# Performance work log

Hardware: AMD Instinct MI355X
Metric: run time of the kernel (lower is better)

Reference implementation:

```python
import jax, jax.numpy as jnp
import numpy as np

C, INTER, RED4 = 256, 128, 64  # in_channels, inter_ch=max(C//2,32), C//4

def setup_inputs() -> dict:
    key = jax.random.key(0)
    ks = jax.random.split(key, 12)
    B, H, W = 8, 64, 64
    s = 0.02
    return {
        "x": jax.random.normal(ks[0], (B, C, H, W), dtype=jnp.float32),
        "theta_w": jax.random.normal(ks[1], (INTER, C), dtype=jnp.float32) * s,
        "phi_w": jax.random.normal(ks[2], (INTER, C), dtype=jnp.float32) * s,
        "g_w": jax.random.normal(ks[3], (INTER, C), dtype=jnp.float32) * s,
        "out_w": jax.random.normal(ks[4], (C, INTER), dtype=jnp.float32) * s,
        "bn_gamma": jnp.ones((C,), dtype=jnp.float32),
        "bn_beta": jnp.zeros((C,), dtype=jnp.float32),
        "fc1_w": jax.random.normal(ks[5], (RED4, C), dtype=jnp.float32) * s,
        "fc1_b": jnp.zeros((RED4,), dtype=jnp.float32),
        "fc2_w": jax.random.normal(ks[6], (C, RED4), dtype=jnp.float32) * s,
        "fc2_b": jnp.zeros((C,), dtype=jnp.float32),
    }

def reference(x, theta_w, phi_w, g_w, out_w, bn_gamma, bn_beta, fc1_w, fc1_b, fc2_w, fc2_b):
    B, Cc, H, W = x.shape
    N = H * W
    xf = x.reshape(B, Cc, N)                              # [B,C,N]
    # 1x1 convs == per-pixel matmuls
    theta = jnp.einsum('ic,bcn->bni', theta_w, xf)        # [B,N,I]
    phi = jnp.einsum('ic,bcn->bin', phi_w, xf)            # [B,I,N]
    g = jnp.einsum('ic,bcn->bni', g_w, xf)                # [B,N,I]
    scale = 1.0 / jnp.sqrt(jnp.asarray(theta.shape[-1], theta.dtype))
    attn = jax.nn.softmax(jnp.einsum('bni,bim->bnm', theta, phi) * scale, axis=-1)  # [B,N,N]
    out = jnp.einsum('bnm,bmi->bni', attn, g)             # [B,N,I]
    out = jnp.einsum('ci,bni->bcn', out_w, out).reshape(B, Cc, H, W)
    # BatchNorm2d (training mode: batch stats, biased variance, eps=1e-5)
    mean = out.mean(axis=(0, 2, 3))
    var = out.var(axis=(0, 2, 3))
    out = (out - mean[:, None, None]) * jax.lax.rsqrt(var[:, None, None] + 1e-5)
    out = out * bn_gamma[:, None, None] + bn_beta[:, None, None]
    # SE channel attention on the input x
    pooled = x.mean(axis=(2, 3))                          # [B,C]
    h = jax.nn.relu(pooled @ fc1_w.T + fc1_b)
    ch_w = jax.nn.sigmoid(h @ fc2_w.T + fc2_b)[:, :, None, None]
    return x + out * ch_w
```

## Files before the change

### kernel.cpp

```cpp
#include <hip/hip_runtime.h>

#define B_DIM 8
#define C_DIM 256
#define I_DIM 128
#define N_DIM 4096
#define R_DIM 64

typedef unsigned short u16;
typedef unsigned int u32;
typedef __attribute__((ext_vector_type(8))) __bf16 bf16x8;
typedef __attribute__((ext_vector_type(4))) float f32x4;
typedef __attribute__((ext_vector_type(16))) float f32x16;

union BF8 { u32 u[4]; bf16x8 v; };

__device__ __forceinline__ u16 f2bf(float f) {
    union { float f; u32 u; } v; v.f = f;
    u32 r = v.u + 0x7FFFu + ((v.u >> 16) & 1u);
    return (u16)(r >> 16);
}
__device__ __forceinline__ float bf2f(u16 h) {
    union { u32 u; float f; } v; v.u = (u32)h << 16; return v.f;
}
__device__ __forceinline__ u32 pk2(float a, float b) {
    return (u32)f2bf(a) | ((u32)f2bf(b) << 16);
}
__device__ __forceinline__ u32 pk2t(float a, float b) {
    union { float f; u32 u; } ua, ub; ua.f = a; ub.f = b;
    return __builtin_amdgcn_perm(ub.u, ua.u, 0x07060302u);
}
__device__ __forceinline__ void async16(const u16* g, u16* l) {
    __builtin_amdgcn_global_load_lds((const __attribute__((address_space(1))) void*)g,
                                     (__attribute__((address_space(3))) void*)l, 16, 0, 0);
}
__device__ __forceinline__ void plswap(u32& a, u32& b) {
    __asm__("v_permlane32_swap_b32 %0, %1" : "+v"(a), "+v"(b));
}

#define TH_SCALE 0.1275204890136f

static constexpr size_t OFF_BNSUM = 0;
static constexpr size_t OFF_BNSQ  = 1024;
static constexpr size_t OFF_POOL  = 2048;
static constexpr size_t OFF_CHW   = 10240;
static constexpr size_t OFF_W3    = 18432;
static constexpr size_t OFF_OWB   = 215040;
static constexpr size_t OFF_AO0   = 280576;
static constexpr size_t OFF_AO1   = OFF_AO0 + 8388608;
static constexpr size_t OFF_THETA = OFF_AO1 + 8388608;
static constexpr size_t OFF_PHIT  = OFF_THETA + 8388608;
static constexpr size_t OFF_GT    = OFF_PHIT + 8388608;
static constexpr size_t OFF_L0    = OFF_GT + 8388608;
static constexpr size_t OFF_L1    = OFF_L0 + 131072;
static constexpr size_t OFF_OUT2  = OFF_L1 + 131072;

__global__ void prep_kernel(const float* __restrict__ tw, const float* __restrict__ pw,
                            const float* __restrict__ gw, const float* __restrict__ ow,
                            u16* __restrict__ w3, u16* __restrict__ owb,
                            float* __restrict__ bnzero, float* __restrict__ pooled) {
    int idx = blockIdx.x * 256 + threadIdx.x;
    if (idx < 512) bnzero[idx] = 0.f;
    if (idx < 2048) pooled[idx] = 0.f;
    if (idx < 3 * 32768) {
        const float* src = idx < 32768 ? tw : (idx < 65536 ? pw : gw);
        w3[idx] = f2bf(src[idx & 32767]);
    }
    if (idx < 32768) owb[idx] = f2bf(ow[idx]);
}

__global__ __launch_bounds__(256) void qkv_kernel(const float* __restrict__ x,
                                                  const u16* __restrict__ w3,
                                                  u16* __restrict__ theta,
                                                  u16* __restrict__ phiT,
                                                  u16* __restrict__ gT,
                                                  float* __restrict__ pooled) {
    const int bid = blockIdx.x;
    const int b = bid & 7, nt = bid >> 3;
    const int n0 = nt * 64;
    const int t = threadIdx.x, lane = t & 63, w = t >> 6;
    const int cl = lane & 31, h = lane >> 5;

    __shared__ u16 As[64 * 256];
    __shared__ u16 Ep[128 * 72];

    {
        const float* xb = x + ((size_t)b * C_DIM) * N_DIM + n0;
        for (int it = 0; it < 16; ++it) {
            int id = it * 256 + t;
            int c = id >> 4, l16 = id & 15;
            float4 v = *(const float4*)(xb + (size_t)c * N_DIM + l16 * 4);
            int g = c >> 3, co = c & 7;
            float vv[4] = {v.x, v.y, v.z, v.w};
            #pragma unroll
            for (int k = 0; k < 4; ++k) {
                int n = l16 * 4 + k;
                As[n * 256 + ((g ^ (n & 7)) << 3) + co] = f2bf(vv[k]);
            }
            float s = (v.x + v.y) + (v.z + v.w);
            s += __shfl_xor(s, 1); s += __shfl_xor(s, 2);
            s += __shfl_xor(s, 4); s += __shfl_xor(s, 8);
            if ((t & 15) == 0) atomicAdd(&pooled[b * C_DIM + c], s);
        }
    }
    __syncthreads();

    const int mt = w & 1;
    const int ip = w >> 1;
    bf16x8 afr[16];
    #pragma unroll
    for (int ks = 0; ks < 16; ++ks) {
        int r = mt * 32 + cl;
        int g = 2 * ks + h;
        afr[ks] = *(const bf16x8*)&As[r * 256 + ((g ^ (r & 7)) << 3)];
    }

    for (int z = 0; z < 3; ++z) {
        const u16* wz = w3 + z * (I_DIM * C_DIM);
        f32x16 acc[2] = {};
        #pragma unroll
        for (int ks = 0; ks < 16; ++ks) {
            #pragma unroll
            for (int f = 0; f < 2; ++f) {
                int irow = (2 * ip + f) * 32 + cl;
                bf16x8 bfr = *(const bf16x8*)(wz + (size_t)irow * C_DIM + ks * 16 + h * 8);
                acc[f] = __builtin_amdgcn_mfma_f32_32x32x16_bf16(afr[ks], bfr, acc[f], 0, 0, 0);
            }
        }
        if (z < 2) {
            float sc = (z == 0) ? TH_SCALE : 1.0f;
            #pragma unroll
            for (int f = 0; f < 2; ++f) {
                int i = (2 * ip + f) * 32 + cl;
                #pragma unroll
                for (int r2 = 0; r2 < 4; ++r2)
                    #pragma unroll
                    for (int e = 0; e < 4; ++e) {
                        int n = mt * 32 + 8 * r2 + 4 * h + e;
                        Ep[n * 136 + i] = f2bf(acc[f][4 * r2 + e] * sc);
                    }
            }
            __syncthreads();
            u16* dst = (z == 0) ? theta : phiT;
            #pragma unroll
            for (int it = 0; it < 4; ++it) {
                int id = it * 256 + t;
                int n = id >> 4, l16 = id & 15;
                f32x4 vv = *(const f32x4*)&Ep[n * 136 + l16 * 8];
                *(f32x4*)(dst + ((size_t)(b * N_DIM) + n0 + n) * I_DIM + l16 * 8) = vv;
            }
            __syncthreads();
        } else {
            #pragma unroll
            for (int f = 0; f < 2; ++f) {
                int i = (2 * ip + f) * 32 + cl;
                #pragma unroll
                for (int r2 = 0; r2 < 4; ++r2) {
                    u32 lo = pk2(acc[f][4 * r2 + 0], acc[f][4 * r2 + 1]);
                    u32 hi = pk2(acc[f][4 * r2 + 2], acc[f][4 * r2 + 3]);
                    int nb = mt * 32 + 8 * r2 + 4 * h;
                    *(u32*)&Ep[i * 72 + nb] = lo;
                    *(u32*)&Ep[i * 72 + nb + 2] = hi;
                }
            }
            __syncthreads();
            #pragma unroll
            for (int it = 0; it < 4; ++it) {
                int id = it * 256 + t;
                int i = id >> 3, l8 = id & 7;
                f32x4 vv = *(const f32x4*)&Ep[i * 72 + l8 * 8];
                *(f32x4*)(gT + ((size_t)(b * I_DIM) + i) * N_DIM + n0 + l8 * 8) = vv;
            }
        }
    }
}

__global__ __launch_bounds__(512, 2) void attn_kernel(const u16* __restrict__ theta,
                                                      const u16* __restrict__ phiT,
                                                      const u16* __restrict__ gT,
                                                      u16* __restrict__ ao0, u16* __restrict__ ao1,
                                                      float* __restrict__ l0, float* __restrict__ l1,
                                                      const float* __restrict__ pooled,
                                                      const float* __restrict__ fc1w,
                                                      const float* __restrict__ fc1b,
                                                      const float* __restrict__ fc2w,
                                                      const float* __restrict__ fc2b,
                                                      float* __restrict__ chw) {
    const int bid = blockIdx.x;
    const int b = bid & 7, mh = (bid >> 3) & 1, qt = bid >> 4;
    const int t = threadIdx.x, lane = t & 63, w = t >> 6;
    const int cl = lane & 31, h = lane >> 5;
    const int wt = w & 3, kh = w >> 2;
    const int qw = qt * 128 + wt * 32;

    __shared__ __align__(16) u16 SM[34816];
    __shared__ float lexs[8][32];
    __shared__ float sse[512];

    bf16x8 qf[8];
    {
        const u16* qp = theta + ((size_t)(b * N_DIM) + qw + cl) * I_DIM + h * 8;
        #pragma unroll
        for (int ks = 0; ks < 8; ++ks) qf[ks] = *(const bf16x8*)(qp + ks * 16);
    }

    const u16* kbase = phiT + (size_t)b * N_DIM * I_DIM + (size_t)(mh * 2048) * I_DIM;
    const u16* vbase = gT + (size_t)b * I_DIM * N_DIM + mh * 2048;
    const u16* kptr[2]; const u16* vptr[2];
    #pragma unroll
    for (int it = 0; it < 2; ++it) {
        int gi = (w * 2 + it) * 64 + lane;
        int kr = gi >> 4, kg = gi & 15;
        kptr[it] = kbase + (size_t)kr * I_DIM + ((kg ^ (kr & 7)) << 3);
        int vr = gi >> 3, vg = gi & 7;
        vptr[it] = vbase + (size_t)vr * N_DIM + ((vg ^ (vr & 7)) << 3);
    }

    auto issue = [&](int p) {
        u16* Kd = SM + p * 16384;
        u16* Vd = Kd + 8192;
        #pragma unroll
        for (int it = 0; it < 2; ++it) { async16(kptr[it], Kd + (w * 2 + it) * 512); kptr[it] += 64 * I_DIM; }
        #pragma unroll
        for (int it = 0; it < 2; ++it) { async16(vptr[it], Vd + (w * 2 + it) * 512); vptr[it] += 64; }
    };

    float lsum = 0.f;
    f32x16 O[4] = {};
    const int krow = kh * 32 + cl;
    const int kswz = krow & 7;

    issue(0);

    for (int mc = 0; mc < 32; ++mc) {
        const int p = mc & 1;
        __asm__ volatile("s_barrier" ::: "memory");
        if (mc < 31) {
            issue(1 - p);
            __asm__ volatile("s_waitcnt vmcnt(4)" ::: "memory");
        } else {
            __asm__ volatile("s_waitcnt vmcnt(0)" ::: "memory");
        }
        __asm__ volatile("s_barrier" ::: "memory");

        const u16* Ks = SM + p * 16384;
        const u16* Vs = Ks + 8192;

        f32x16 S = {};
        __builtin_amdgcn_s_setprio(1);
        #pragma unroll
        for (int ks = 0; ks < 8; ++ks) {
            bf16x8 kf = *(const bf16x8*)&Ks[krow * 128 + (((2 * ks + h) ^ kswz) << 3)];
            S = __builtin_amdgcn_mfma_f32_32x32x16_bf16(kf, qf[ks], S, 0, 0, 0);
        }
        __builtin_amdgcn_s_setprio(0);

        u32 pk[4][2];
        #pragma unroll
        for (int r2 = 0; r2 < 4; ++r2) {
            float p0 = __builtin_amdgcn_exp2f(S[4 * r2 + 0]);
            float p1 = __builtin_amdgcn_exp2f(S[4 * r2 + 1]);
            float p2 = __builtin_amdgcn_exp2f(S[4 * r2 + 2]);
            float p3 = __builtin_amdgcn_exp2f(S[4 * r2 + 3]);
            lsum += (p0 + p1) + (p2 + p3);
            pk[r2][0] = pk2t(p0, p1);
            pk[r2][1] = pk2t(p2, p3);
        }

        __builtin_amdgcn_s_setprio(1);
        #pragma unroll
        for (int s = 0; s < 2; ++s) {
            u32 x0 = pk[2 * s][0], y0 = pk[2 * s + 1][0];
            u32 x1 = pk[2 * s][1], y1 = pk[2 * s + 1][1];
            plswap(x0, y0);
            plswap(x1, y1);
            BF8 A;
            A.u[0] = x0; A.u[1] = x1; A.u[2] = y0; A.u[3] = y1;
            const int g = 4 * kh + 2 * s + h;
            #pragma unroll
            for (int f = 0; f < 4; ++f) {
                int ir = f * 32 + cl;
                bf16x8 vf = *(const bf16x8*)&Vs[ir * 64 + ((g ^ (ir & 7)) << 3)];
                O[f] = __builtin_amdgcn_mfma_f32_32x32x16_bf16(A.v, vf, O[f], 0, 0, 0);
            }
        }
        __builtin_amdgcn_s_setprio(0);
    }

    {
        union { float f; u32 u; } a, b2;
        a.f = lsum; b2.f = lsum;
        plswap(a.u, b2.u);
        lsum = a.f + b2.f;
    }
    if (h == 0) lexs[w][cl] = lsum;
    __syncthreads();

    float* ep32 = (float*)SM;
    float* slot = ep32 + ((wt << 6) + lane) * 68;
    if (kh == 0) {
        #pragma unroll
        for (int f = 0; f < 4; ++f)
            #pragma unroll
            for (int r2 = 0; r2 < 4; ++r2) {
                f32x4 vv = {O[f][4 * r2 + 0], O[f][4 * r2 + 1], O[f][4 * r2 + 2], O[f][4 * r2 + 3]};
                *(f32x4*)(slot + f * 16 + r2 * 4) = vv;
            }
    }
    __syncthreads();

    u16* aop = (mh == 0) ? ao0 : ao1;
    float* lp = (mh == 0) ? l0 : l1;

    if (kh == 1) {
        if (h == 0) lp[(size_t)b * N_DIM + qw + cl] = lexs[wt][cl] + lexs[wt + 4][cl];
        float linv[16];
        #pragma unroll
        for (int r2 = 0; r2 < 4; ++r2) {
            f32x4 la = *(const f32x4*)&lexs[wt][8 * r2 + 4 * h];
            f32x4 lb = *(const f32x4*)&lexs[wt + 4][8 * r2 + 4 * h];
            #pragma unroll
            for (int e = 0; e < 4; ++e) linv[4 * r2 + e] = 1.f / (la[e] + lb[e]);
        }
        #pragma unroll
        for (int f = 0; f < 4; ++f)
            #pragma unroll
            for (int r2 = 0; r2 < 4; ++r2) {
                f32x4 pv = *(const f32x4*)(slot + f * 16 + r2 * 4);
                #pragma unroll
                for (int e = 0; e < 4; ++e)
                    O[f][4 * r2 + e] = (O[f][4 * r2 + e] + pv[e]) * linv[4 * r2 + e];
            }
    }
    __syncthreads();

    if (kh == 1) {
        u16* ep = SM + wt * 4096;
        #pragma unroll
        for (int f = 0; f < 4; ++f)
            #pragma unroll
            for (int r2 = 0; r2 < 4; ++r2)
                #pragma unroll
                for (int e = 0; e < 4; ++e) {
                    int q = 8 * r2 + 4 * h + e;
                    ep[q * 128 + f * 32 + cl] = f2bf(O[f][4 * r2 + e]);
                }
        __asm__ volatile("s_waitcnt lgkmcnt(0)" ::: "memory");
        #pragma unroll
        for (int it = 0; it < 8; ++it) {
            int id = it * 64 + lane;
            int q = id >> 4, l16 = id & 15;
            f32x4 vv = *(const f32x4*)&ep[q * 128 + l16 * 8];
            *(f32x4*)(aop + ((size_t)(b * N_DIM) + qw + q) * I_DIM + l16 * 8) = vv;
        }
    }

    if (bid == 0) {
        const int sb = t >> 6;
        const int j = t & 63;
        float d = 0.f;
        for (int c = 0; c < C_DIM; c += 4) {
            float4 pv = *(const float4*)(pooled + sb * C_DIM + c);
            float4 wv = *(const float4*)(fc1w + j * C_DIM + c);
            d += (pv.x * wv.x + pv.y * wv.y) + (pv.z * wv.z + pv.w * wv.w);
        }
        float a = fc1b[j] + d * (1.f / N_DIM);
        sse[sb * 64 + j] = a > 0.f ? a : 0.f;
        __syncthreads();
        #pragma unroll
        for (int r = 0; r < 4; ++r) {
            int c = j * 4 + r;
            float acc = fc2b[c];
            for (int k = 0; k < R_DIM; k += 4) {
                float4 wv = *(const float4*)(fc2w + c * 64 + k);
                acc += (sse[sb * 64 + k] * wv.x + sse[sb * 64 + k + 1] * wv.y)
                     + (sse[sb * 64 + k + 2] * wv.z + sse[sb * 64 + k + 3] * wv.w);
            }
            chw[sb * C_DIM + c] = 1.f / (1.f + __builtin_amdgcn_exp2f(-acc * 1.44269504089f));
        }
    }
}

__global__ __launch_bounds__(256) void oproj_kernel(const u16* __restrict__ ao0,
                                                    const u16* __restrict__ ao1,
                                                    const float* __restrict__ l0,
                                                    const float* __restrict__ l1,
                                                    const u16* __restrict__ owb,
                                                    u16* __restrict__ out2,
                                                    float* __restrict__ bnsum,
                                                    float* __restrict__ bnsumsq) {
    const int bid = blockIdx.x;
    const int b = bid & 7, nt = bid >> 3;
    const int n0 = nt * 64;
    const int t = threadIdx.x, lane = t & 63, w = t >> 6;
    const int cl = lane & 31, h = lane >> 5;

    __shared__ u16 Ep[256 * 72];
    __shared__ float lsum[C_DIM], lsq[C_DIM];
    lsum[t] = 0.f; lsq[t] = 0.f;
    __syncthreads();

    const int mt = w & 1;
    const int nn = n0 + mt * 32 + cl;
    float w0, w1;
    {
        float la = l0[(size_t)b * N_DIM + nn], lb = l1[(size_t)b * N_DIM + nn];
        float inv = 1.f / (la + lb);
        w0 = la * inv; w1 = lb * inv;
    }
    bf16x8 afr[8];
    {
        const u16* p0 = ao0 + ((size_t)(b * N_DIM) + nn) * I_DIM + h * 8;
        const u16* p1 = ao1 + ((size_t)(b * N_DIM) + nn) * I_DIM + h * 8;
        #pragma unroll
        for (int ks = 0; ks < 8; ++ks) {
            bf16x8 x0 = *(const bf16x8*)(p0 + ks * 16);
            bf16x8 x1 = *(const bf16x8*)(p1 + ks * 16);
            const u16* u0 = (const u16*)&x0;
            const u16* u1 = (const u16*)&x1;
            float c0 = w0 * bf2f(u0[0]) + w1 * bf2f(u1[0]);
            float c1 = w0 * bf2f(u0[1]) + w1 * bf2f(u1[1]);
            float c2 = w0 * bf2f(u0[2]) + w1 * bf2f(u1[2]);
            float c3 = w0 * bf2f(u0[3]) + w1 * bf2f(u1[3]);
            float c4 = w0 * bf2f(u0[4]) + w1 * bf2f(u1[4]);
            float c5 = w0 * bf2f(u0[5]) + w1 * bf2f(u1[5]);
            float c6 = w0 * bf2f(u0[6]) + w1 * bf2f(u1[6]);
            float c7 = w0 * bf2f(u0[7]) + w1 * bf2f(u1[7]);
            BF8 r;
            r.u[0] = pk2(c0, c1); r.u[1] = pk2(c2, c3);
            r.u[2] = pk2(c4, c5); r.u[3] = pk2(c6, c7);
            afr[ks] = r.v;
        }
    }

    f32x16 D[4] = {};
    #pragma unroll
    for (int ks = 0; ks < 8; ++ks) {
        #pragma unroll
        for (int j = 0; j < 4; ++j) {
            int cr = ((w >> 1) * 4 + j) * 32 + cl;
            bf16x8 bfr = *(const bf16x8*)(owb + (size_t)cr * I_DIM + ks * 16 + h * 8);
            D[j] = __builtin_amdgcn_mfma_f32_32x32x16_bf16(afr[ks], bfr, D[j], 0, 0, 0);
        }
    }

    #pragma unroll
    for (int j = 0; j < 4; ++j) {
        int c = ((w >> 1) * 4 + j) * 32 + cl;
        float s1 = 0.f, s2 = 0.f;
        #pragma unroll
        for (int r2 = 0; r2 < 4; ++r2) {
            float v0 = D[j][4 * r2 + 0], v1 = D[j][4 * r2 + 1];
            float v2 = D[j][4 * r2 + 2], v3 = D[j][4 * r2 + 3];
            s1 += (v0 + v1) + (v2 + v3);
            s2 += (v0 * v0 + v1 * v1) + (v2 * v2 + v3 * v3);
            int nb = mt * 32 + 8 * r2 + 4 * h;
            *(u32*)&Ep[c * 72 + nb] = pk2(v0, v1);
            *(u32*)&Ep[c * 72 + nb + 2] = pk2(v2, v3);
        }
        atomicAdd(&lsum[c], s1);
        atomicAdd(&lsq[c], s2);
    }
    __syncthreads();
    #pragma unroll
    for (int it = 0; it < 8; ++it) {
        int id = it * 256 + t;
        int c = id >> 3, l8 = id & 7;
        f32x4 vv = *(const f32x4*)&Ep[c * 72 + l8 * 8];
        *(f32x4*)(out2 + ((size_t)(b * C_DIM) + c) * N_DIM + n0 + l8 * 8) = vv;
    }
    atomicAdd(&bnsum[t], lsum[t]);
    atomicAdd(&bnsumsq[t], lsq[t]);
}

__global__ void final_kernel(const float* __restrict__ x, const u16* __restrict__ out2,
                             const float* __restrict__ bnsum, const float* __restrict__ bnsumsq,
                             const float* __restrict__ gamma, const float* __restrict__ beta,
                             const float* __restrict__ chw, float* __restrict__ out) {
    int idx = blockIdx.x * 256 + threadIdx.x;
    int e = idx * 4;
    int b = e >> 20;
    int c = (e >> 12) & 255;
    float mean = bnsum[c] * (1.f / 32768.f);
    float var = bnsumsq[c] * (1.f / 32768.f) - mean * mean;
    float sc = gamma[c] * rsqrtf(var + 1e-5f);
    float sh = beta[c] - mean * sc;
    float cw = chw[b * C_DIM + c];
    ushort4 o16 = ((const ushort4*)out2)[idx];
    float4 xv = ((const float4*)x)[idx];
    float4 res;
    res.x = xv.x + (bf2f(o16.x) * sc + sh) * cw;
    res.y = xv.y + (bf2f(o16.y) * sc + sh) * cw;
    res.z = xv.z + (bf2f(o16.z) * sc + sh) * cw;
    res.w = xv.w + (bf2f(o16.w) * sc + sh) * cw;
    ((float4*)out)[idx] = res;
}

extern "C" void kernel_launch(void* const* d_in, const int* in_sizes, int n_in,
                              void* d_out, int out_size, void* d_ws, size_t ws_size,
                              hipStream_t stream) {
    const float* x   = (const float*)d_in[0];
    const float* tw  = (const float*)d_in[1];
    const float* pw  = (const float*)d_in[2];
    const float* gw  = (const float*)d_in[3];
    const float* ow  = (const float*)d_in[4];
    const float* gam = (const float*)d_in[5];
    const float* bet = (const float*)d_in[6];
    const float* f1w = (const float*)d_in[7];
    const float* f1b = (const float*)d_in[8];
    const float* f2w = (const float*)d_in[9];
    const float* f2b = (const float*)d_in[10];
    float* out = (float*)d_out;

    char* ws = (char*)d_ws;
    float* bnsum   = (float*)(ws + OFF_BNSUM);
    float* bnsumsq = (float*)(ws + OFF_BNSQ);
    float* pooled  = (float*)(ws + OFF_POOL);
    float* chw     = (float*)(ws + OFF_CHW);
    u16*   w3      = (u16*)(ws + OFF_W3);
    u16*   owb     = (u16*)(ws + OFF_OWB);
    u16*   ao0     = (u16*)(ws + OFF_AO0);
    u16*   ao1     = (u16*)(ws + OFF_AO1);
    u16*   theta   = (u16*)(ws + OFF_THETA);
    u16*   phiT    = (u16*)(ws + OFF_PHIT);
    u16*   gT      = (u16*)(ws + OFF_GT);
    float* l0      = (float*)(ws + OFF_L0);
    float* l1      = (float*)(ws + OFF_L1);
    u16*   out2    = (u16*)(ws + OFF_OUT2);

    prep_kernel<<<384, 256, 0, stream>>>(tw, pw, gw, ow, w3, owb, bnsum, pooled);
    qkv_kernel<<<512, 256, 0, stream>>>(x, w3, theta, phiT, gT, pooled);
    attn_kernel<<<512, 512, 0, stream>>>(theta, phiT, gT, ao0, ao1, l0, l1,
                                         pooled, f1w, f1b, f2w, f2b, chw);
    oproj_kernel<<<512, 256, 0, stream>>>(ao0, ao1, l0, l1, owb, out2, bnsum, bnsumsq);
    final_kernel<<<8192, 256, 0, stream>>>(x, out2, bnsum, bnsumsq, gam, bet, chw, out);
}
```

Measured before the change: 299.3 us.

## Give each attention wave two query tiles and drop the split-key reduction

After: 298.3 us. About the same (-0.3%).

```diff
diff --git a/kernel.cpp b/kernel.cpp
--- a/kernel.cpp
+++ b/kernel.cpp
@@ -174,7 +174,7 @@
     }
 }
 
-__global__ __launch_bounds__(512, 2) void attn_kernel(const u16* __restrict__ theta,
+__global__ __launch_bounds__(256, 1) void attn_kernel(const u16* __restrict__ theta,
                                                       const u16* __restrict__ phiT,
                                                       const u16* __restrict__ gT,
                                                       u16* __restrict__ ao0, u16* __restrict__ ao1,
@@ -189,26 +189,26 @@
     const int b = bid & 7, mh = (bid >> 3) & 1, qt = bid >> 4;
     const int t = threadIdx.x, lane = t & 63, w = t >> 6;
     const int cl = lane & 31, h = lane >> 5;
-    const int wt = w & 3, kh = w >> 2;
-    const int qw = qt * 128 + wt * 32;
-
-    __shared__ __align__(16) u16 SM[34816];
-    __shared__ float lexs[8][32];
+    const int qw = qt * 256 + w * 64;
+
+    __shared__ __align__(16) u16 SM[32768];
+    __shared__ float lexw[4][2][32];
     __shared__ float sse[512];
 
-    bf16x8 qf[8];
-    {
-        const u16* qp = theta + ((size_t)(b * N_DIM) + qw + cl) * I_DIM + h * 8;
-        #pragma unroll
-        for (int ks = 0; ks < 8; ++ks) qf[ks] = *(const bf16x8*)(qp + ks * 16);
+    bf16x8 qf[2][8];
+    #pragma unroll
+    for (int qs = 0; qs < 2; ++qs) {
+        const u16* qp = theta + ((size_t)(b * N_DIM) + qw + qs * 32 + cl) * I_DIM + h * 8;
+        #pragma unroll
+        for (int ks = 0; ks < 8; ++ks) qf[qs][ks] = *(const bf16x8*)(qp + ks * 16);
     }
 
     const u16* kbase = phiT + (size_t)b * N_DIM * I_DIM + (size_t)(mh * 2048) * I_DIM;
     const u16* vbase = gT + (size_t)b * I_DIM * N_DIM + mh * 2048;
-    const u16* kptr[2]; const u16* vptr[2];
-    #pragma unroll
-    for (int it = 0; it < 2; ++it) {
-        int gi = (w * 2 + it) * 64 + lane;
+    const u16* kptr[4]; const u16* vptr[4];
+    #pragma unroll
+    for (int it = 0; it < 4; ++it) {
+        int gi = (w * 4 + it) * 64 + lane;
         int kr = gi >> 4, kg = gi & 15;
         kptr[it] = kbase + (size_t)kr * I_DIM + ((kg ^ (kr & 7)) << 3);
         int vr = gi >> 3, vg = gi & 7;
@@ -219,15 +219,13 @@
         u16* Kd = SM + p * 16384;
         u16* Vd = Kd + 8192;
         #pragma unroll
-        for (int it = 0; it < 2; ++it) { async16(kptr[it], Kd + (w * 2 + it) * 512); kptr[it] += 64 * I_DIM; }
-        #pragma unroll
-        for (int it = 0; it < 2; ++it) { async16(vptr[it], Vd + (w * 2 + it) * 512); vptr[it] += 64; }
+        for (int it = 0; it < 4; ++it) { async16(kptr[it], Kd + (w * 4 + it) * 512); kptr[it] += 64 * I_DIM; }
+        #pragma unroll
+        for (int it = 0; it < 4; ++it) { async16(vptr[it], Vd + (w * 4 + it) * 512); vptr[it] += 64; }
     };
 
-    float lsum = 0.f;
-    f32x16 O[4] = {};
-    const int krow = kh * 32 + cl;
-    const int kswz = krow & 7;
+    float lsum0 = 0.f, lsum1 = 0.f;
+    f32x16 O0[4] = {}, O1[4] = {};
 
     issue(0);
 
@@ -236,7 +234,7 @@
         __asm__ volatile("s_barrier" ::: "memory");
         if (mc < 31) {
             issue(1 - p);
-            __asm__ volatile("s_waitcnt vmcnt(4)" ::: "memory");
+            __asm__ volatile("s_waitcnt vmcnt(8)" ::: "memory");
         } else {
             __asm__ volatile("s_waitcnt vmcnt(0)" ::: "memory");
         }
@@ -245,96 +243,97 @@
         const u16* Ks = SM + p * 16384;
         const u16* Vs = Ks + 8192;
 
-        f32x16 S = {};
-        __builtin_amdgcn_s_setprio(1);
-        #pragma unroll
-        for (int ks = 0; ks < 8; ++ks) {
-            bf16x8 kf = *(const bf16x8*)&Ks[krow * 128 + (((2 * ks + h) ^ kswz) << 3)];
-            S = __builtin_amdgcn_mfma_f32_32x32x16_bf16(kf, qf[ks], S, 0, 0, 0);
-        }
-        __builtin_amdgcn_s_setprio(0);
-
-        u32 pk[4][2];
-        #pragma unroll
-        for (int r2 = 0; r2 < 4; ++r2) {
-            float p0 = __builtin_amdgcn_exp2f(S[4 * r2 + 0]);
-            float p1 = __builtin_amdgcn_exp2f(S[4 * r2 + 1]);
-            float p2 = __builtin_amdgcn_exp2f(S[4 * r2 + 2]);
-            float p3 = __builtin_amdgcn_exp2f(S[4 * r2 + 3]);
-            lsum += (p0 + p1) + (p2 + p3);
-            pk[r2][0] = pk2t(p0, p1);
-            pk[r2][1] = pk2t(p2, p3);
-        }
-
-        __builtin_amdgcn_s_setprio(1);
-        #pragma unroll
-        for (int s = 0; s < 2; ++s) {
-            u32 x0 = pk[2 * s][0], y0 = pk[2 * s + 1][0];
-            u32 x1 = pk[2 * s][1], y1 = pk[2 * s + 1][1];
-            plswap(x0, y0);
-            plswap(x1, y1);
-            BF8 A;
-            A.u[0] = x0; A.u[1] = x1; A.u[2] = y0; A.u[3] = y1;
-            const int g = 4 * kh + 2 * s + h;
-            #pragma unroll
-            for (int f = 0; f < 4; ++f) {
-                int ir = f * 32 + cl;
-                bf16x8 vf = *(const bf16x8*)&Vs[ir * 64 + ((g ^ (ir & 7)) << 3)];
-                O[f] = __builtin_amdgcn_mfma_f32_32x32x16_bf16(A.v, vf, O[f], 0, 0, 0);
-            }
-        }
-        __builtin_amdgcn_s_setprio(0);
+        #pragma unroll
+        for (int kt = 0; kt < 2; ++kt) {
+            f32x16 S0 = {}, S1 = {};
+            __builtin_amdgcn_s_setprio(1);
+            #pragma unroll
+            for (int ks = 0; ks < 8; ++ks) {
+                int r = kt * 32 + cl;
+                bf16x8 kf = *(const bf16x8*)&Ks[r * 128 + (((2 * ks + h) ^ (r & 7)) << 3)];
+                S0 = __builtin_amdgcn_mfma_f32_32x32x16_bf16(kf, qf[0][ks], S0, 0, 0, 0);
+                S1 = __builtin_amdgcn_mfma_f32_32x32x16_bf16(kf, qf[1][ks], S1, 0, 0, 0);
+            }
+            __builtin_amdgcn_s_setprio(0);
+
+            u32 pk0[4][2], pk1[4][2];
+            #pragma unroll
+            for (int r2 = 0; r2 < 4; ++r2) {
+                float a0 = __builtin_amdgcn_exp2f(S0[4 * r2 + 0]);
+                float a1 = __builtin_amdgcn_exp2f(S0[4 * r2 + 1]);
+                float a2 = __builtin_amdgcn_exp2f(S0[4 * r2 + 2]);
+                float a3 = __builtin_amdgcn_exp2f(S0[4 * r2 + 3]);
+                lsum0 += (a0 + a1) + (a2 + a3);
+                pk0[r2][0] = pk2t(a0, a1);
+                pk0[r2][1] = pk2t(a2, a3);
+                float b0 = __builtin_amdgcn_exp2f(S1[4 * r2 + 0]);
+                float b1 = __builtin_amdgcn_exp2f(S1[4 * r2 + 1]);
+                float b2 = __builtin_amdgcn_exp2f(S1[4 * r2 + 2]);
+                float b3 = __builtin_amdgcn_exp2f(S1[4 * r2 + 3]);
+                lsum1 += (b0 + b1) + (b2 + b3);
+                pk1[r2][0] = pk2t(b0, b1);
+                pk1[r2][1] = pk2t(b2, b3);
+            }
+
+            __builtin_amdgcn_s_setprio(1);
+            #pragma unroll
+            for (int s = 0; s < 2; ++s) {
+                u32 x0 = pk0[2 * s][0], y0 = pk0[2 * s + 1][0];
+                u32 x1 = pk0[2 * s][1], y1 = pk0[2 * s + 1][1];
+                plswap(x0, y0);
+                plswap(x1, y1);
+                BF8 A0; A0.u[0] = x0; A0.u[1] = x1; A0.u[2] = y0; A0.u[3] = y1;
+                u32 m0 = pk1[2 * s][0], n0_ = pk1[2 * s + 1][0];
+                u32 m1 = pk1[2 * s][1], n1_ = pk1[2 * s + 1][1];
+                plswap(m0, n0_);
+                plswap(m1, n1_);
+                BF8 A1; A1.u[0] = m0; A1.u[1] = m1; A1.u[2] = n0_; A1.u[3] = n1_;
+                const int g = kt * 4 + 2 * s + h;
+                #pragma unroll
+                for (int f = 0; f < 4; ++f) {
+                    int ir = f * 32 + cl;
+                    bf16x8 vf = *(const bf16x8*)&Vs[ir * 64 + ((g ^ (ir & 7)) << 3)];
+                    O0[f] = __builtin_amdgcn_mfma_f32_32x32x16_bf16(A0.v, vf, O0[f], 0, 0, 0);
+                    O1[f] = __builtin_amdgcn_mfma_f32_32x32x16_bf16(A1.v, vf, O1[f], 0, 0, 0);
+                }
+            }
+            __builtin_amdgcn_s_setprio(0);
+        }
     }
 
     {
         union { float f; u32 u; } a, b2;
-        a.f = lsum; b2.f = lsum;
+        a.f = lsum0; b2.f = lsum0;
         plswap(a.u, b2.u);
-        lsum = a.f + b2.f;
-    }
-    if (h == 0) lexs[w][cl] = lsum;
-    __syncthreads();
-
-    float* ep32 = (float*)SM;
-    float* slot = ep32 + ((wt << 6) + lane) * 68;
-    if (kh == 0) {
-        #pragma unroll
-        for (int f = 0; f < 4; ++f)
-            #pragma unroll
-            for (int r2 = 0; r2 < 4; ++r2) {
-                f32x4 vv = {O[f][4 * r2 + 0], O[f][4 * r2 + 1], O[f][4 * r2 + 2], O[f][4 * r2 + 3]};
-                *(f32x4*)(slot + f * 16 + r2 * 4) = vv;
-            }
-    }
+        lsum0 = a.f + b2.f;
+        a.f = lsum1; b2.f = lsum1;
+        plswap(a.u, b2.u);
+        lsum1 = a.f + b2.f;
+    }
+    if (h == 0) { lexw[w][0][cl] = lsum0; lexw[w][1][cl] = lsum1; }
     __syncthreads();
 
     u16* aop = (mh == 0) ? ao0 : ao1;
     float* lp = (mh == 0) ? l0 : l1;
-
-    if (kh == 1) {
-        if (h == 0) lp[(size_t)b * N_DIM + qw + cl] = lexs[wt][cl] + lexs[wt + 4][cl];
+    if (h == 0) {
+        lp[(size_t)b * N_DIM + qw + cl] = lsum0;
+        lp[(size_t)b * N_DIM + qw + 32 + cl] = lsum1;
+    }
+
+    u16* ep = SM + w * 8192;
+    #pragma unroll
+    for (int qs = 0; qs < 2; ++qs) {
         float linv[16];
-        #pragma unroll
-        for (int r2 = 0; r2 < 4; ++r2) {
-            f32x4 la = *(const f32x4*)&lexs[wt][8 * r2 + 4 * h];
-            f32x4 lb = *(const f32x4*)&lexs[wt + 4][8 * r2 + 4 * h];
-            #pragma unroll
-            for (int e = 0; e < 4; ++e) linv[4 * r2 + e] = 1.f / (la[e] + lb[e]);
-        }
-        #pragma unroll
-        for (int f = 0; f < 4; ++f)
+        {
+            float* lw = lexw[w][qs];
             #pragma unroll
             for (int r2 = 0; r2 < 4; ++r2) {
-                f32x4 pv = *(const f32x4*)(slot + f * 16 + r2 * 4);
+                f32x4 lv = *(const f32x4*)&lw[8 * r2 + 4 * h];
                 #pragma unroll
-                for (int e = 0; e < 4; ++e)
-                    O[f][4 * r2 + e] = (O[f][4 * r2 + e] + pv[e]) * linv[4 * r2 + e];
-            }
-    }
-    __syncthreads();
-
-    if (kh == 1) {
-        u16* ep = SM + wt * 4096;
+                for (int e = 0; e < 4; ++e) linv[4 * r2 + e] = 1.f / lv[e];
+            }
+        }
+        u16* e2 = ep + qs * 4096;
         #pragma unroll
         for (int f = 0; f < 4; ++f)
             #pragma unroll
@@ -342,36 +341,41 @@
                 #pragma unroll
                 for (int e = 0; e < 4; ++e) {
                     int q = 8 * r2 + 4 * h + e;
-                    ep[q * 128 + f * 32 + cl] = f2bf(O[f][4 * r2 + e]);
+                    float ov = (qs == 0) ? O0[f][4 * r2 + e] : O1[f][4 * r2 + e];
+                    e2[q * 128 + f * 32 + cl] = f2bf(ov * linv[4 * r2 + e]);
                 }
-        __asm__ volatile("s_waitcnt lgkmcnt(0)" ::: "memory");
-        #pragma unroll
-        for (int it = 0; it < 8; ++it) {
-            int id = it * 64 + lane;
-            int q = id >> 4, l16 = id & 15;
-            f32x4 vv = *(const f32x4*)&ep[q * 128 + l16 * 8];
-            *(f32x4*)(aop + ((size_t)(b * N_DIM) + qw + q) * I_DIM + l16 * 8) = vv;
-        }
+    }
+    __asm__ volatile("s_waitcnt lgkmcnt(0)" ::: "memory");
+    #pragma unroll
+    for (int it = 0; it < 16; ++it) {
+        int id = it * 64 + lane;
+        int q = id >> 4, l16 = id & 15;
+        f32x4 vv = *(const f32x4*)&ep[q * 128 + l16 * 8];
+        *(f32x4*)(aop + ((size_t)(b * N_DIM) + qw + q) * I_DIM + l16 * 8) = vv;
     }
 
     if (bid == 0) {
-        const int sb = t >> 6;
-        const int j = t & 63;
-        float d = 0.f;
-        for (int c = 0; c < C_DIM; c += 4) {
-            float4 pv = *(const float4*)(pooled + sb * C_DIM + c);
-            float4 wv = *(const float4*)(fc1w + j * C_DIM + c);
-            d += (pv.x * wv.x + pv.y * wv.y) + (pv.z * wv.z + pv.w * wv.w);
-        }
-        float a = fc1b[j] + d * (1.f / N_DIM);
-        sse[sb * 64 + j] = a > 0.f ? a : 0.f;
+        const int sb = t >> 5;
+        #pragma unroll
+        for (int pp = 0; pp < 2; ++pp) {
+            int j = (t & 31) + pp * 32;
+            float d = 0.f;
+            for (int c = 0; c < C_DIM; c += 4) {
+                float4 pv = *(const float4*)(pooled + sb * C_DIM + c);
+                float4 wv = *(const float4*)(fc1w + j * C_DIM + c);
+                d += (pv.x * wv.x + pv.y * wv.y) + (pv.z * wv.z + pv.w * wv.w);
+            }
+            float a = fc1b[j] + d * (1.f / N_DIM);
+            sse[sb * 64 + j] = a > 0.f ? a : 0.f;
+        }
         __syncthreads();
-        #pragma unroll
-        for (int r = 0; r < 4; ++r) {
-            int c = j * 4 + r;
+        const int c0 = (t & 31) * 8;
+        #pragma unroll
+        for (int r = 0; r < 8; ++r) {
+            int c = c0 + r;
             float acc = fc2b[c];
             for (int k = 0; k < R_DIM; k += 4) {
-                float4 wv = *(const float4*)(fc2w + c * 64 + k);
+                float4 wv = *(const float4*)(fc2w + c * R_DIM + k);
                 acc += (sse[sb * 64 + k] * wv.x + sse[sb * 64 + k + 1] * wv.y)
                      + (sse[sb * 64 + k + 2] * wv.z + sse[sb * 64 + k + 3] * wv.w);
             }
@@ -529,7 +533,7 @@
 
     prep_kernel<<<384, 256, 0, stream>>>(tw, pw, gw, ow, w3, owb, bnsum, pooled);
     qkv_kernel<<<512, 256, 0, stream>>>(x, w3, theta, phiT, gT, pooled);
-    attn_kernel<<<512, 512, 0, stream>>>(theta, phiT, gT, ao0, ao1, l0, l1,
+    attn_kernel<<<256, 256, 0, stream>>>(theta, phiT, gT, ao0, ao1, l0, l1,
                                          pooled, f1w, f1b, f2w, f2b, chw);
     oproj_kernel<<<512, 256, 0, stream>>>(ao0, ao1, l0, l1, owb, out2, bnsum, bnsumsq);
     final_kernel<<<8192, 256, 0, stream>>>(x, out2, bnsum, bnsumsq, gam, bet, chw, out);
```
